# Optimization experiments

Measured on AMD Instinct MI355X. Metric: run time of the kernel, lower is better.

## Reference

```python
import jax, jax.numpy as jnp
import numpy as np

N = 50000          # nodes
E = 800000         # edges (before self-loops)
F_IN = 500         # input features
H1, C1 = 8, 16     # layer-1 heads, per-head channels
NUM_CLASSES = 7
NEG_SLOPE = 0.2


def setup_inputs() -> dict:
    key = jax.random.key(0)
    ks = jax.random.split(key, 10)
    s = 0.05
    return {
        "x": jax.random.normal(ks[0], (N, F_IN), jnp.float32),
        "edge_index": jax.random.randint(ks[1], (2, E), 0, N, dtype=jnp.int64),
        "W1": jax.random.normal(ks[2], (F_IN, H1 * C1), jnp.float32) * s,
        "att_src1": jax.random.normal(ks[3], (H1, C1), jnp.float32) * s,
        "att_dst1": jax.random.normal(ks[4], (H1, C1), jnp.float32) * s,
        "b1": jnp.zeros((H1 * C1,), jnp.float32),
        "W2": jax.random.normal(ks[5], (H1 * C1, NUM_CLASSES), jnp.float32) * s,
        "att_src2": jax.random.normal(ks[6], (1, NUM_CLASSES), jnp.float32) * s,
        "att_dst2": jax.random.normal(ks[7], (1, NUM_CLASSES), jnp.float32) * s,
        "b2": jnp.zeros((NUM_CLASSES,), jnp.float32),
    }


def _gat_conv(x, W, att_src, att_dst, bias, src, dst, concat):
    # PyG GATConv (eval mode: attention dropout is identity).
    H, C = att_src.shape
    h = (x @ W).reshape(N, H, C)                      # [N,H,C]
    a_src = jnp.sum(h * att_src, axis=-1)             # [N,H]
    a_dst = jnp.sum(h * att_dst, axis=-1)             # [N,H]
    e = a_src[src] + a_dst[dst]                       # [Et,H] per-edge logits
    e = jax.nn.leaky_relu(e, NEG_SLOPE)
    # segment softmax over incoming edges of each destination node
    m = jax.ops.segment_max(e, dst, num_segments=N)   # [N,H]
    e = jnp.exp(e - m[dst])
    denom = jax.ops.segment_sum(e, dst, num_segments=N)  # [N,H]
    alpha = e / (denom[dst] + 1e-16)                  # [Et,H]
    msg = h[src] * alpha[:, :, None]                  # [Et,H,C]
    out = jax.ops.segment_sum(msg, dst, num_segments=N)  # [N,H,C]
    if concat:
        out = out.reshape(N, H * C)
    else:
        out = out.mean(axis=1)
    return out + bias


def reference(x, edge_index, W1, att_src1, att_dst1, b1, W2, att_src2, att_dst2, b2):
    # add self-loops (PyG default add_self_loops=True)
    loops = jnp.arange(N, dtype=edge_index.dtype)
    src = jnp.concatenate([edge_index[0], loops])
    dst = jnp.concatenate([edge_index[1], loops])
    h = _gat_conv(x, W1, att_src1, att_dst1, b1, src, dst, concat=True)
    h = jax.nn.relu(h)
    # F.dropout(p=0.6, training=False) -> identity in eval mode
    out = _gat_conv(h, W2, att_src2, att_dst2, b2, src, dst, concat=False)
    return out
```

## Files before the change

kernel.cpp:

```cpp
#include <hip/hip_runtime.h>
#include <hip/hip_bf16.h>

#define NN 50000
#define EE 800000
#define ETOT 850000
#define FIN 500
#define HC 128
#define NH 8
#define CH 16
#define NC 7

#define OW1  0
#define OAS1 64000
#define OAD1 64128
#define OB1  64256
#define OW2  64384
#define OAS2 65280
#define OAD2 65287
#define OB2  65294
#define WTOT 65301

#define GR1  64
#define GK   32
#define KPAD 512
#define ASTR 40
#define BSTR 40

typedef __hip_bfloat16 bf16;
typedef __attribute__((ext_vector_type(8))) short short8;
typedef __attribute__((ext_vector_type(4))) float f32x4;

__device__ __forceinline__ float b2f(const bf16 v) { return __bfloat162float(v); }
__device__ __forceinline__ float lrelu(float v) { return fmaxf(v, 0.2f * v); }
__device__ __forceinline__ float elog(float v) { return __expf(fminf(lrelu(v), 30.f)); }
__device__ __forceinline__ float blo(unsigned w) { return __uint_as_float(w << 16); }
__device__ __forceinline__ float bhi(unsigned w) { return __uint_as_float(w & 0xffff0000u); }
__device__ __forceinline__ unsigned short f2bu(float f)
{
    bf16 h = __float2bfloat16(f);
    return *(unsigned short*)&h;
}

__device__ __forceinline__ int eread(const void* __restrict__ eidx, long long i, int is64)
{
    if (is64) return (int)((const long long*)eidx)[i];
    return ((const int*)eidx)[i];
}

__global__ void detect_kernel(const unsigned short* __restrict__ xraw,
                              const unsigned int* __restrict__ eraw,
                              int* __restrict__ flags)
{
    __shared__ int s_insane, s_oddnz;
    if (threadIdx.x == 0) { s_insane = 0; s_oddnz = 0; }
    __syncthreads();
    int insane = 0;
    for (int i = threadIdx.x; i < 8192; i += 256) {
        const unsigned int bits = ((unsigned int)xraw[i]) << 16;
        const float v = __uint_as_float(bits);
        const float a = fabsf(v);
        const bool sane = (v == 0.0f) || (a >= 1e-30f && a <= 1e4f);
        if (!sane) insane++;
    }
    int oddnz = 0;
    for (int i = threadIdx.x; i < 512; i += 256) {
        if (eraw[2 * i + 1] != 0u) oddnz++;
    }
    atomicAdd(&s_insane, insane);
    atomicAdd(&s_oddnz, oddnz);
    __syncthreads();
    if (threadIdx.x == 0) {
        flags[0] = (s_insane < 256) ? 1 : 0;
        flags[1] = (s_oddnz == 0) ? 1 : 0;
    }
}

__global__ void conv_w_kernel(const void* W1, const void* as1, const void* ad1, const void* b1,
                              const void* W2, const void* as2, const void* ad2, const void* b2,
                              float* __restrict__ wc, const int* __restrict__ flags)
{
    const int i = blockIdx.x * blockDim.x + threadIdx.x;
    if (i >= WTOT) return;
    const void* src; int off;
    if (i < OAS1)      { src = W1;  off = i - OW1; }
    else if (i < OAD1) { src = as1; off = i - OAS1; }
    else if (i < OB1)  { src = ad1; off = i - OAD1; }
    else if (i < OW2)  { src = b1;  off = i - OB1; }
    else if (i < OAS2) { src = W2;  off = i - OW2; }
    else if (i < OAD2) { src = as2; off = i - OAS2; }
    else if (i < OB2)  { src = ad2; off = i - OAD2; }
    else               { src = b2;  off = i - OB2; }
    float v;
    if (flags[0]) v = b2f(((const bf16*)src)[off]);
    else          v = ((const float*)src)[off];
    wc[i] = v;
}

__global__ void conv_w1t_kernel(const void* __restrict__ W1, unsigned short* __restrict__ w1t,
                                const int* __restrict__ flags)
{
    const int i = blockIdx.x * blockDim.x + threadIdx.x;
    if (i >= HC * KPAD) return;
    const int col = i >> 9;
    const int k   = i & (KPAD - 1);
    float v = 0.f;
    if (k < FIN) {
        if (flags[0]) v = b2f(((const bf16*)W1)[k * HC + col]);
        else          v = ((const float*)W1)[k * HC + col];
    }
    w1t[i] = f2bu(v);
}

__global__ void hist_kernel(const void* __restrict__ eidx, int* __restrict__ deg,
                            const int* __restrict__ flags)
{
    const int e = blockIdx.x * blockDim.x + threadIdx.x;
    if (e >= ETOT) return;
    int d;
    if (e < EE) d = eread(eidx, (long long)EE + e, flags[1]);
    else        d = e - EE;
    if ((unsigned)d < (unsigned)NN) atomicAdd(&deg[d], 1);
}

__global__ void scan_k1_kernel(const int* __restrict__ deg, int* __restrict__ bsum)
{
    __shared__ int lds[256];
    const int i = blockIdx.x * 256 + threadIdx.x;
    lds[threadIdx.x] = (i < NN) ? deg[i] : 0;
    __syncthreads();
    for (int s = 128; s > 0; s >>= 1) {
        if (threadIdx.x < s) lds[threadIdx.x] += lds[threadIdx.x + s];
        __syncthreads();
    }
    if (threadIdx.x == 0) bsum[blockIdx.x] = lds[0];
}

__global__ void scan_k2_kernel(int* __restrict__ bsum)
{
    __shared__ int a[256], b[256], orig[256];
    const int t = threadIdx.x;
    a[t] = bsum[t]; orig[t] = a[t];
    __syncthreads();
    int* cur = a; int* nxt = b;
    for (int off = 1; off < 256; off <<= 1) {
        nxt[t] = cur[t] + ((t >= off) ? cur[t - off] : 0);
        __syncthreads();
        int* tmp = cur; cur = nxt; nxt = tmp;
    }
    bsum[t] = cur[t] - orig[t];
}

__global__ void scan_k3_kernel(const int* __restrict__ deg, const int* __restrict__ bsum,
                               int* __restrict__ rowptr)
{
    __shared__ int a[256], b[256], own[256];
    const int t = threadIdx.x;
    const int i = blockIdx.x * 256 + t;
    const int v = (i < NN) ? deg[i] : 0;
    a[t] = v; own[t] = v;
    __syncthreads();
    int* cur = a; int* nxt = b;
    for (int off = 1; off < 256; off <<= 1) {
        nxt[t] = cur[t] + ((t >= off) ? cur[t - off] : 0);
        __syncthreads();
        int* tmp = cur; cur = nxt; nxt = tmp;
    }
    if (i < NN) rowptr[i] = bsum[blockIdx.x] + cur[t] - own[t];
}

__global__ void scatter_kernel(const void* __restrict__ eidx, int* __restrict__ rowptr,
                               int* __restrict__ esrc_sorted, const int* __restrict__ flags)
{
    const int e = blockIdx.x * blockDim.x + threadIdx.x;
    if (e >= ETOT) return;
    int s, d;
    if (e < EE) {
        s = eread(eidx, e, flags[1]);
        d = eread(eidx, (long long)EE + e, flags[1]);
    } else s = d = e - EE;
    if ((unsigned)s >= (unsigned)NN || (unsigned)d >= (unsigned)NN) return;
    const int pos = atomicAdd(&rowptr[d], 1);
    if ((unsigned)pos < (unsigned)ETOT) esrc_sorted[pos] = s;
}

__global__ __launch_bounds__(256) void gemm1_mfma_kernel(
    const void* __restrict__ x, const unsigned short* __restrict__ w1t,
    bf16* __restrict__ h1, const int* __restrict__ flags)
{
    __shared__ unsigned short Asl[GR1 * ASTR];
    __shared__ unsigned short Bsl[HC * BSTR];

    const int t    = threadIdx.x;
    const int wv   = t >> 6;
    const int lane = t & 63;
    const int m15  = lane & 15;
    const int quad = lane >> 4;
    const int r0   = blockIdx.x * GR1;
    const int isbf = flags[0];
    const float* xf = (const float*)x;
    const bf16*  xb = (const bf16*)x;

    const int wr  = (wv >> 1) * 32;
    const int wcb = (wv & 1) * 64;

    f32x4 acc[2][4];
#pragma unroll
    for (int i = 0; i < 2; ++i)
#pragma unroll
        for (int j = 0; j < 4; ++j) acc[i][j] = (f32x4){0.f, 0.f, 0.f, 0.f};

    const int arow = t >> 2;
    const int akk  = (t & 3) * 8;
    const int bcol = t & 127;
    const int bks  = (t >> 7) * 16;

    for (int kt = 0; kt < 16; ++kt) {
        const int k0 = kt * GK;
        {
            const int grow = r0 + arow;
            if (!isbf && grow < NN && (k0 + akk + 8) <= FIN) {
                const size_t base = (size_t)grow * FIN + k0 + akk;
                const float4 v0 = *(const float4*)(xf + base);
                const float4 v1 = *(const float4*)(xf + base + 4);
                uint4 pk;
                pk.x = (unsigned)f2bu(v0.x) | ((unsigned)f2bu(v0.y) << 16);
                pk.y = (unsigned)f2bu(v0.z) | ((unsigned)f2bu(v0.w) << 16);
                pk.z = (unsigned)f2bu(v1.x) | ((unsigned)f2bu(v1.y) << 16);
                pk.w = (unsigned)f2bu(v1.z) | ((unsigned)f2bu(v1.w) << 16);
                *(uint4*)&Asl[arow * ASTR + akk] = pk;
            } else {
#pragma unroll
                for (int j = 0; j < 8; ++j) {
                    const int k = k0 + akk + j;
                    float v = 0.f;
                    if (grow < NN && k < FIN)
                        v = isbf ? b2f(xb[(size_t)grow * FIN + k]) : xf[(size_t)grow * FIN + k];
                    Asl[arow * ASTR + akk + j] = f2bu(v);
                }
            }
        }
        {
            const unsigned short* gp = w1t + (size_t)bcol * KPAD + k0 + bks;
            *(uint4*)&Bsl[bcol * BSTR + bks]     = *(const uint4*)gp;
            *(uint4*)&Bsl[bcol * BSTR + bks + 8] = *(const uint4*)(gp + 8);
        }
        __syncthreads();

        const int ak = quad * 8;
        const short8 a0 = *(const short8*)&Asl[(wr + m15) * ASTR + ak];
        const short8 a1 = *(const short8*)&Asl[(wr + 16 + m15) * ASTR + ak];
#pragma unroll
        for (int ct = 0; ct < 4; ++ct) {
            const short8 b = *(const short8*)&Bsl[(wcb + ct * 16 + m15) * BSTR + ak];
            acc[0][ct] = __builtin_amdgcn_mfma_f32_16x16x32_bf16(a0, b, acc[0][ct], 0, 0, 0);
            acc[1][ct] = __builtin_amdgcn_mfma_f32_16x16x32_bf16(a1, b, acc[1][ct], 0, 0, 0);
        }
        __syncthreads();
    }

#pragma unroll
    for (int rt = 0; rt < 2; ++rt) {
#pragma unroll
        for (int reg = 0; reg < 4; ++reg) {
            const int row = r0 + wr + rt * 16 + quad * 4 + reg;
            if (row < NN) {
                bf16* hp = h1 + (size_t)row * HC;
#pragma unroll
                for (int ct = 0; ct < 4; ++ct)
                    hp[wcb + ct * 16 + m15] = __float2bfloat16(acc[rt][ct][reg]);
            }
        }
    }
}

__global__ void att1_kernel(const bf16* __restrict__ h1, const float* __restrict__ wc,
                            float* __restrict__ a_src, float* __restrict__ a_dst)
{
    const int idx = blockIdx.x * blockDim.x + threadIdx.x;
    if (idx >= NN * NH) return;
    const int h = idx & 7;
    const unsigned int* hp = (const unsigned int*)(h1 + (size_t)(idx >> 3) * HC + h * CH);
    float s = 0.f, d = 0.f;
#pragma unroll
    for (int u = 0; u < 8; ++u) {
        const unsigned int w = hp[u];
        s += blo(w) * wc[OAS1 + h * CH + 2 * u] + bhi(w) * wc[OAS1 + h * CH + 2 * u + 1];
        d += blo(w) * wc[OAD1 + h * CH + 2 * u] + bhi(w) * wc[OAD1 + h * CH + 2 * u + 1];
    }
    a_src[idx] = s;
    a_dst[idx] = d;
}

__global__ __launch_bounds__(256) void gather1_kernel(
    const int* __restrict__ rowptr, const int* __restrict__ esrc_sorted,
    const float* __restrict__ a_src, const float* __restrict__ a_dst,
    const bf16* __restrict__ h1, float* __restrict__ out1)
{
    const int node = blockIdx.x * 4 + (threadIdx.x >> 6);
    if (node >= NN) return;
    const int lane = threadIdx.x & 63;
    const int h = lane >> 3;
    const float ad = a_dst[node * NH + h];
    const int start = (node == 0) ? 0 : rowptr[node - 1];
    const int end   = rowptr[node];
    float acc0 = 0.f, acc1 = 0.f, den = 0.f;
    int i = start;
    for (; i + 4 <= end; i += 4) {
        const int s0 = esrc_sorted[i + 0];
        const int s1 = esrc_sorted[i + 1];
        const int s2 = esrc_sorted[i + 2];
        const int s3 = esrc_sorted[i + 3];
        const float e0 = a_src[s0 * NH + h];
        const float e1 = a_src[s1 * NH + h];
        const float e2 = a_src[s2 * NH + h];
        const float e3 = a_src[s3 * NH + h];
        const unsigned w0 = *(const unsigned*)(h1 + (size_t)s0 * HC + 2 * lane);
        const unsigned w1 = *(const unsigned*)(h1 + (size_t)s1 * HC + 2 * lane);
        const unsigned w2 = *(const unsigned*)(h1 + (size_t)s2 * HC + 2 * lane);
        const unsigned w3 = *(const unsigned*)(h1 + (size_t)s3 * HC + 2 * lane);
        const float n0 = elog(e0 + ad);
        const float n1 = elog(e1 + ad);
        const float n2 = elog(e2 + ad);
        const float n3 = elog(e3 + ad);
        acc0 += n0 * blo(w0) + n1 * blo(w1) + n2 * blo(w2) + n3 * blo(w3);
        acc1 += n0 * bhi(w0) + n1 * bhi(w1) + n2 * bhi(w2) + n3 * bhi(w3);
        den  += n0 + n1 + n2 + n3;
    }
    for (; i < end; ++i) {
        const int s = esrc_sorted[i];
        const float num = elog(a_src[s * NH + h] + ad);
        const unsigned w = *(const unsigned*)(h1 + (size_t)s * HC + 2 * lane);
        acc0 += num * blo(w);
        acc1 += num * bhi(w);
        den  += num;
    }
    const float inv = 1.f / (den + 1e-16f);
    float* op = out1 + (size_t)node * HC + 2 * lane;
    op[0] = acc0 * inv;
    op[1] = acc1 * inv;
}

__global__ __launch_bounds__(256) void gemm2_kernel(
    const float* __restrict__ out1, const float* __restrict__ wc, float* __restrict__ h2)
{
    __shared__ float W2s[HC * NC];
    __shared__ float B1s[HC];
    for (int i = threadIdx.x; i < HC * NC; i += 256) W2s[i] = wc[OW2 + i];
    if (threadIdx.x < HC) B1s[threadIdx.x] = wc[OB1 + threadIdx.x];
    __syncthreads();
    const int nl = threadIdx.x >> 3;
    const int c  = threadIdx.x & 7;
    const int node = blockIdx.x * 32 + nl;
    if (c >= NC || node >= NN) return;
    const float* hp = out1 + (size_t)node * HC;
    float acc = 0.f;
#pragma unroll
    for (int k4 = 0; k4 < 32; ++k4) {
        const float4 hv = *(const float4*)&hp[4 * k4];
        acc += fmaxf(hv.x + B1s[4 * k4 + 0], 0.f) * W2s[(4 * k4 + 0) * NC + c];
        acc += fmaxf(hv.y + B1s[4 * k4 + 1], 0.f) * W2s[(4 * k4 + 1) * NC + c];
        acc += fmaxf(hv.z + B1s[4 * k4 + 2], 0.f) * W2s[(4 * k4 + 2) * NC + c];
        acc += fmaxf(hv.w + B1s[4 * k4 + 3], 0.f) * W2s[(4 * k4 + 3) * NC + c];
    }
    h2[node * NC + c] = acc;
}

__global__ void att2_kernel(const float* __restrict__ h2, const float* __restrict__ wc,
                            float* __restrict__ a_src, float* __restrict__ a_dst)
{
    const int n = blockIdx.x * blockDim.x + threadIdx.x;
    if (n >= NN) return;
    float s = 0.f, d = 0.f;
#pragma unroll
    for (int c = 0; c < NC; ++c) {
        const float hv = h2[n * NC + c];
        s += hv * wc[OAS2 + c];
        d += hv * wc[OAD2 + c];
    }
    a_src[n] = s;
    a_dst[n] = d;
}

__global__ __launch_bounds__(256) void gather2_kernel(
    const int* __restrict__ rowptr, const int* __restrict__ esrc_sorted,
    const float* __restrict__ a_src, const float* __restrict__ a_dst,
    const float* __restrict__ h2, const float* __restrict__ wc,
    void* __restrict__ out, const int* __restrict__ flags)
{
    const int node = blockIdx.x * 32 + (threadIdx.x >> 3);
    if (node >= NN) return;
    const int c = threadIdx.x & 7;
    const float ad = a_dst[node];
    const int start = (node == 0) ? 0 : rowptr[node - 1];
    const int end   = rowptr[node];
    const int cc = (c < NC) ? c : 0;
    float acc = 0.f, den = 0.f;
    int i = start;
    for (; i + 4 <= end; i += 4) {
        const int s0 = esrc_sorted[i + 0];
        const int s1 = esrc_sorted[i + 1];
        const int s2 = esrc_sorted[i + 2];
        const int s3 = esrc_sorted[i + 3];
        const float e0 = a_src[s0];
        const float e1 = a_src[s1];
        const float e2 = a_src[s2];
        const float e3 = a_src[s3];
        const float v0 = h2[s0 * NC + cc];
        const float v1 = h2[s1 * NC + cc];
        const float v2 = h2[s2 * NC + cc];
        const float v3 = h2[s3 * NC + cc];
        const float n0 = elog(e0 + ad);
        const float n1 = elog(e1 + ad);
        const float n2 = elog(e2 + ad);
        const float n3 = elog(e3 + ad);
        acc += n0 * v0 + n1 * v1 + n2 * v2 + n3 * v3;
        den += n0 + n1 + n2 + n3;
    }
    for (; i < end; ++i) {
        const int s = esrc_sorted[i];
        const float num = elog(a_src[s] + ad);
        den += num;
        acc += num * h2[s * NC + cc];
    }
    if (c >= NC) return;
    const float v = acc / (den + 1e-16f) + wc[OB2 + c];
    if (flags[0]) ((bf16*)out)[node * NC + c] = __float2bfloat16(v);
    else          ((float*)out)[node * NC + c] = v;
}

extern "C" void kernel_launch(void* const* d_in, const int* in_sizes, int n_in,
                              void* d_out, int out_size, void* d_ws, size_t ws_size,
                              hipStream_t stream)
{
    const void* x        = d_in[0];
    const void* eidx     = d_in[1];
    const void* W1       = d_in[2];
    const void* att_src1 = d_in[3];
    const void* att_dst1 = d_in[4];
    const void* b1       = d_in[5];
    const void* W2       = d_in[6];
    const void* att_src2 = d_in[7];
    const void* att_dst2 = d_in[8];
    const void* b2       = d_in[9];

    float* ws = (float*)d_ws;
    size_t o = 0;
    int*   flags  = (int*)(ws + o);            o += 16;
    float* wc     = ws + o;                    o += 65312;
    unsigned short* w1t = (unsigned short*)(ws + o); o += (HC * KPAD) / 2;
    int*   deg    = (int*)(ws + o);            o += 50000;
    int*   rowptr = (int*)(ws + o);            o += 50016;
    int*   bsum   = (int*)(ws + o);            o += 256;
    int*   esrt   = (int*)(ws + o);            o += 850000;
    bf16*  h1     = (bf16*)(ws + o);           o += (size_t)NN * HC / 2;
    float* a_src1 = ws + o;                    o += (size_t)NN * NH;
    float* a_dst1 = ws + o;                    o += (size_t)NN * NH;
    float* out1   = ws + o;                    o += (size_t)NN * HC;
    float* h2     = ws + o;                    o += (size_t)NN * NC;
    float* a_src2 = ws + o;                    o += NN;
    float* a_dst2 = ws + o;                    o += NN;

    detect_kernel<<<1, 256, 0, stream>>>((const unsigned short*)x, (const unsigned int*)eidx, flags);
    conv_w_kernel<<<(WTOT + 255) / 256, 256, 0, stream>>>(W1, att_src1, att_dst1, b1,
                                                          W2, att_src2, att_dst2, b2, wc, flags);
    conv_w1t_kernel<<<(HC * KPAD + 255) / 256, 256, 0, stream>>>(W1, w1t, flags);
    hipMemsetAsync(deg, 0, (size_t)NN * sizeof(int), stream);
    hist_kernel<<<(ETOT + 255) / 256, 256, 0, stream>>>(eidx, deg, flags);
    scan_k1_kernel<<<(NN + 255) / 256, 256, 0, stream>>>(deg, bsum);
    scan_k2_kernel<<<1, 256, 0, stream>>>(bsum);
    scan_k3_kernel<<<(NN + 255) / 256, 256, 0, stream>>>(deg, bsum, rowptr);
    scatter_kernel<<<(ETOT + 255) / 256, 256, 0, stream>>>(eidx, rowptr, esrt, flags);

    gemm1_mfma_kernel<<<(NN + GR1 - 1) / GR1, 256, 0, stream>>>(x, w1t, h1, flags);
    att1_kernel<<<(NN * NH + 255) / 256, 256, 0, stream>>>(h1, wc, a_src1, a_dst1);
    gather1_kernel<<<(NN + 3) / 4, 256, 0, stream>>>(rowptr, esrt, a_src1, a_dst1, h1, out1);
    gemm2_kernel<<<(NN + 31) / 32, 256, 0, stream>>>(out1, wc, h2);
    att2_kernel<<<(NN + 255) / 256, 256, 0, stream>>>(h2, wc, a_src2, a_dst2);
    gather2_kernel<<<(NN + 31) / 32, 256, 0, stream>>>(rowptr, esrt, a_src2, a_dst2, h2, wc, d_out, flags);
}
```

Baseline: 382.6 us.

## Reuse histogram atomic ranks for scatter, unroll gather1, fuse att2 into gemm2

The histogram pass stores each edge's atomic return value as its rank within its destination, so scatter computes the position as rowptr plus rank without atomics, and rowptr becomes an exclusive prefix with a sentinel end. The layer-1 gather loop is unrolled to eight edges to keep more independent loads in flight. The layer-2 attention projection is computed inside gemm2 via lane shuffles, removing a kernel launch and a reread of h2. The cost is an extra per-edge rank array that must be written and read.

```diff
diff --git a/kernel.cpp b/kernel.cpp
--- a/kernel.cpp
+++ b/kernel.cpp
@@ -49,7 +49,7 @@
 
 __global__ void detect_kernel(const unsigned short* __restrict__ xraw,
                               const unsigned int* __restrict__ eraw,
-                              int* __restrict__ flags)
+                              int* __restrict__ flags, int* __restrict__ rowptr)
 {
     __shared__ int s_insane, s_oddnz;
     if (threadIdx.x == 0) { s_insane = 0; s_oddnz = 0; }
@@ -72,6 +72,7 @@
     if (threadIdx.x == 0) {
         flags[0] = (s_insane < 256) ? 1 : 0;
         flags[1] = (s_oddnz == 0) ? 1 : 0;
+        rowptr[NN] = ETOT;
     }
 }
 
@@ -112,14 +113,16 @@
 }
 
 __global__ void hist_kernel(const void* __restrict__ eidx, int* __restrict__ deg,
-                            const int* __restrict__ flags)
+                            int* __restrict__ rank, const int* __restrict__ flags)
 {
     const int e = blockIdx.x * blockDim.x + threadIdx.x;
     if (e >= ETOT) return;
     int d;
     if (e < EE) d = eread(eidx, (long long)EE + e, flags[1]);
     else        d = e - EE;
-    if ((unsigned)d < (unsigned)NN) atomicAdd(&deg[d], 1);
+    int r = -1;
+    if ((unsigned)d < (unsigned)NN) r = atomicAdd(&deg[d], 1);
+    rank[e] = r;
 }
 
 __global__ void scan_k1_kernel(const int* __restrict__ deg, int* __restrict__ bsum)
@@ -168,8 +171,9 @@
     if (i < NN) rowptr[i] = bsum[blockIdx.x] + cur[t] - own[t];
 }
 
-__global__ void scatter_kernel(const void* __restrict__ eidx, int* __restrict__ rowptr,
-                               int* __restrict__ esrc_sorted, const int* __restrict__ flags)
+__global__ void scatter_kernel(const void* __restrict__ eidx, const int* __restrict__ rowptr,
+                               const int* __restrict__ rank, int* __restrict__ esrc_sorted,
+                               const int* __restrict__ flags)
 {
     const int e = blockIdx.x * blockDim.x + threadIdx.x;
     if (e >= ETOT) return;
@@ -179,7 +183,9 @@
         d = eread(eidx, (long long)EE + e, flags[1]);
     } else s = d = e - EE;
     if ((unsigned)s >= (unsigned)NN || (unsigned)d >= (unsigned)NN) return;
-    const int pos = atomicAdd(&rowptr[d], 1);
+    const int r = rank[e];
+    if (r < 0) return;
+    const int pos = rowptr[d] + r;
     if ((unsigned)pos < (unsigned)ETOT) esrc_sorted[pos] = s;
 }
 
@@ -301,30 +307,27 @@
     const int lane = threadIdx.x & 63;
     const int h = lane >> 3;
     const float ad = a_dst[node * NH + h];
-    const int start = (node == 0) ? 0 : rowptr[node - 1];
-    const int end   = rowptr[node];
+    const int start = rowptr[node];
+    const int end   = rowptr[node + 1];
     float acc0 = 0.f, acc1 = 0.f, den = 0.f;
     int i = start;
-    for (; i + 4 <= end; i += 4) {
-        const int s0 = esrc_sorted[i + 0];
-        const int s1 = esrc_sorted[i + 1];
-        const int s2 = esrc_sorted[i + 2];
-        const int s3 = esrc_sorted[i + 3];
-        const float e0 = a_src[s0 * NH + h];
-        const float e1 = a_src[s1 * NH + h];
-        const float e2 = a_src[s2 * NH + h];
-        const float e3 = a_src[s3 * NH + h];
-        const unsigned w0 = *(const unsigned*)(h1 + (size_t)s0 * HC + 2 * lane);
-        const unsigned w1 = *(const unsigned*)(h1 + (size_t)s1 * HC + 2 * lane);
-        const unsigned w2 = *(const unsigned*)(h1 + (size_t)s2 * HC + 2 * lane);
-        const unsigned w3 = *(const unsigned*)(h1 + (size_t)s3 * HC + 2 * lane);
-        const float n0 = elog(e0 + ad);
-        const float n1 = elog(e1 + ad);
-        const float n2 = elog(e2 + ad);
-        const float n3 = elog(e3 + ad);
-        acc0 += n0 * blo(w0) + n1 * blo(w1) + n2 * blo(w2) + n3 * blo(w3);
-        acc1 += n0 * bhi(w0) + n1 * bhi(w1) + n2 * bhi(w2) + n3 * bhi(w3);
-        den  += n0 + n1 + n2 + n3;
+    for (; i + 8 <= end; i += 8) {
+        int   sv[8];
+        float ev[8];
+        unsigned wv[8];
+#pragma unroll
+        for (int j = 0; j < 8; ++j) sv[j] = esrc_sorted[i + j];
+#pragma unroll
+        for (int j = 0; j < 8; ++j) ev[j] = a_src[sv[j] * NH + h];
+#pragma unroll
+        for (int j = 0; j < 8; ++j) wv[j] = *(const unsigned*)(h1 + (size_t)sv[j] * HC + 2 * lane);
+#pragma unroll
+        for (int j = 0; j < 8; ++j) {
+            const float n = elog(ev[j] + ad);
+            acc0 += n * blo(wv[j]);
+            acc1 += n * bhi(wv[j]);
+            den  += n;
+        }
     }
     for (; i < end; ++i) {
         const int s = esrc_sorted[i];
@@ -341,7 +344,8 @@
 }
 
 __global__ __launch_bounds__(256) void gemm2_kernel(
-    const float* __restrict__ out1, const float* __restrict__ wc, float* __restrict__ h2)
+    const float* __restrict__ out1, const float* __restrict__ wc, float* __restrict__ h2,
+    float* __restrict__ a_src2, float* __restrict__ a_dst2)
 {
     __shared__ float W2s[HC * NC];
     __shared__ float B1s[HC];
@@ -351,34 +355,31 @@
     const int nl = threadIdx.x >> 3;
     const int c  = threadIdx.x & 7;
     const int node = blockIdx.x * 32 + nl;
-    if (c >= NC || node >= NN) return;
-    const float* hp = out1 + (size_t)node * HC;
+    const bool valid = (node < NN) && (c < NC);
     float acc = 0.f;
-#pragma unroll
-    for (int k4 = 0; k4 < 32; ++k4) {
-        const float4 hv = *(const float4*)&hp[4 * k4];
-        acc += fmaxf(hv.x + B1s[4 * k4 + 0], 0.f) * W2s[(4 * k4 + 0) * NC + c];
-        acc += fmaxf(hv.y + B1s[4 * k4 + 1], 0.f) * W2s[(4 * k4 + 1) * NC + c];
-        acc += fmaxf(hv.z + B1s[4 * k4 + 2], 0.f) * W2s[(4 * k4 + 2) * NC + c];
-        acc += fmaxf(hv.w + B1s[4 * k4 + 3], 0.f) * W2s[(4 * k4 + 3) * NC + c];
-    }
-    h2[node * NC + c] = acc;
-}
-
-__global__ void att2_kernel(const float* __restrict__ h2, const float* __restrict__ wc,
-                            float* __restrict__ a_src, float* __restrict__ a_dst)
-{
-    const int n = blockIdx.x * blockDim.x + threadIdx.x;
-    if (n >= NN) return;
-    float s = 0.f, d = 0.f;
-#pragma unroll
-    for (int c = 0; c < NC; ++c) {
-        const float hv = h2[n * NC + c];
-        s += hv * wc[OAS2 + c];
-        d += hv * wc[OAD2 + c];
-    }
-    a_src[n] = s;
-    a_dst[n] = d;
+    if (valid) {
+        const float* hp = out1 + (size_t)node * HC;
+#pragma unroll
+        for (int k4 = 0; k4 < 32; ++k4) {
+            const float4 hv = *(const float4*)&hp[4 * k4];
+            acc += fmaxf(hv.x + B1s[4 * k4 + 0], 0.f) * W2s[(4 * k4 + 0) * NC + c];
+            acc += fmaxf(hv.y + B1s[4 * k4 + 1], 0.f) * W2s[(4 * k4 + 1) * NC + c];
+            acc += fmaxf(hv.z + B1s[4 * k4 + 2], 0.f) * W2s[(4 * k4 + 2) * NC + c];
+            acc += fmaxf(hv.w + B1s[4 * k4 + 3], 0.f) * W2s[(4 * k4 + 3) * NC + c];
+        }
+        h2[node * NC + c] = acc;
+    }
+    float ps = valid ? acc * wc[OAS2 + c] : 0.f;
+    float pd = valid ? acc * wc[OAD2 + c] : 0.f;
+#pragma unroll
+    for (int m = 1; m < 8; m <<= 1) {
+        ps += __shfl_xor(ps, m, 8);
+        pd += __shfl_xor(pd, m, 8);
+    }
+    if (node < NN && c == 0) {
+        a_src2[node] = ps;
+        a_dst2[node] = pd;
+    }
 }
 
 __global__ __launch_bounds__(256) void gather2_kernel(
@@ -391,8 +392,8 @@
     if (node >= NN) return;
     const int c = threadIdx.x & 7;
     const float ad = a_dst[node];
-    const int start = (node == 0) ? 0 : rowptr[node - 1];
-    const int end   = rowptr[node];
+    const int start = rowptr[node];
+    const int end   = rowptr[node + 1];
     const int cc = (c < NC) ? c : 0;
     float acc = 0.f, den = 0.f;
     int i = start;
@@ -452,6 +453,7 @@
     int*   rowptr = (int*)(ws + o);            o += 50016;
     int*   bsum   = (int*)(ws + o);            o += 256;
     int*   esrt   = (int*)(ws + o);            o += 850000;
+    int*   rank   = (int*)(ws + o);            o += 850000;
     bf16*  h1     = (bf16*)(ws + o);           o += (size_t)NN * HC / 2;
     float* a_src1 = ws + o;                    o += (size_t)NN * NH;
     float* a_dst1 = ws + o;                    o += (size_t)NN * NH;
@@ -460,21 +462,21 @@
     float* a_src2 = ws + o;                    o += NN;
     float* a_dst2 = ws + o;                    o += NN;
 
-    detect_kernel<<<1, 256, 0, stream>>>((const unsigned short*)x, (const unsigned int*)eidx, flags);
+    detect_kernel<<<1, 256, 0, stream>>>((const unsigned short*)x, (const unsigned int*)eidx,
+                                         flags, rowptr);
     conv_w_kernel<<<(WTOT + 255) / 256, 256, 0, stream>>>(W1, att_src1, att_dst1, b1,
                                                           W2, att_src2, att_dst2, b2, wc, flags);
     conv_w1t_kernel<<<(HC * KPAD + 255) / 256, 256, 0, stream>>>(W1, w1t, flags);
     hipMemsetAsync(deg, 0, (size_t)NN * sizeof(int), stream);
-    hist_kernel<<<(ETOT + 255) / 256, 256, 0, stream>>>(eidx, deg, flags);
+    hist_kernel<<<(ETOT + 255) / 256, 256, 0, stream>>>(eidx, deg, rank, flags);
     scan_k1_kernel<<<(NN + 255) / 256, 256, 0, stream>>>(deg, bsum);
     scan_k2_kernel<<<1, 256, 0, stream>>>(bsum);
     scan_k3_kernel<<<(NN + 255) / 256, 256, 0, stream>>>(deg, bsum, rowptr);
-    scatter_kernel<<<(ETOT + 255) / 256, 256, 0, stream>>>(eidx, rowptr, esrt, flags);
+    scatter_kernel<<<(ETOT + 255) / 256, 256, 0, stream>>>(eidx, rowptr, rank, esrt, flags);
 
     gemm1_mfma_kernel<<<(NN + GR1 - 1) / GR1, 256, 0, stream>>>(x, w1t, h1, flags);
     att1_kernel<<<(NN * NH + 255) / 256, 256, 0, stream>>>(h1, wc, a_src1, a_dst1);
     gather1_kernel<<<(NN + 3) / 4, 256, 0, stream>>>(rowptr, esrt, a_src1, a_dst1, h1, out1);
-    gemm2_kernel<<<(NN + 31) / 32, 256, 0, stream>>>(out1, wc, h2);
-    att2_kernel<<<(NN + 255) / 256, 256, 0, stream>>>(h2, wc, a_src2, a_dst2);
+    gemm2_kernel<<<(NN + 31) / 32, 256, 0, stream>>>(out1, wc, h2, a_src2, a_dst2);
     gather2_kernel<<<(NN + 31) / 32, 256, 0, stream>>>(rowptr, esrt, a_src2, a_dst2, h2, wc, d_out, flags);
 }
```

Measured after the change: 339.8 us. -11.2%, faster.
